# Performance work log

Hardware: AMD Instinct MI355X
Metric: run time of the kernel (lower is better)

## Reference

```python
import jax, jax.numpy as jnp
import numpy as np
from jax import lax

D_MODEL = 512
D_STATE = 16
D_CONV = 4
EXPAND = 2
D_INNER = EXPAND * D_MODEL          # 1024
DT_RANK = int(np.ceil(D_MODEL / 16))  # 32


def setup_inputs() -> dict:
    key = jax.random.key(0)
    ks = jax.random.split(key, 10)
    s = lambda k, shape, sc: (jax.random.normal(k, shape, dtype=jnp.float32) * sc)
    x = jax.random.normal(ks[0], (8, D_MODEL, 128, 128), dtype=jnp.float32)
    W_in = s(ks[1], (2 * D_INNER, D_MODEL), 1.0 / np.sqrt(D_MODEL))
    conv_w = s(ks[2], (D_INNER, D_CONV), 1.0 / np.sqrt(D_CONV))
    conv_b = s(ks[3], (D_INNER,), 0.02)
    W_x = s(ks[4], (DT_RANK + 2 * D_STATE, D_INNER), 1.0 / np.sqrt(D_INNER))
    W_dt = s(ks[5], (D_INNER, DT_RANK), 1.0 / np.sqrt(DT_RANK))
    b_dt = s(ks[6], (D_INNER,), 0.02)
    # S4D-real init: A_log[d, n] = log(n+1)
    A_log = jnp.log(jnp.broadcast_to(jnp.arange(1, D_STATE + 1, dtype=jnp.float32), (D_INNER, D_STATE)))
    D_param = jnp.ones((D_INNER,), dtype=jnp.float32)
    W_out = s(ks[7], (D_MODEL, D_INNER), 1.0 / np.sqrt(D_INNER))
    return {"x": x, "W_in": W_in, "conv_w": conv_w, "conv_b": conv_b,
            "W_x": W_x, "W_dt": W_dt, "b_dt": b_dt, "A_log": A_log,
            "D_param": D_param, "W_out": W_out}


def _mamba(u, W_in, conv_w, conv_b, W_x, W_dt, b_dt, A_log, D_param, W_out):
    # u: (B, L, D_MODEL)
    B, L, _ = u.shape
    xz = jnp.einsum('bld,ed->ble', u, W_in)          # (B, L, 2*D_INNER)
    xp, z = jnp.split(xz, 2, axis=-1)                # each (B, L, D_INNER)
    # causal depthwise conv1d over L
    xc = lax.conv_general_dilated(
        xp.transpose(0, 2, 1), conv_w[:, None, :],
        window_strides=(1,), padding=((D_CONV - 1, 0),),
        dimension_numbers=('NCH', 'OIH', 'NCH'),
        feature_group_count=D_INNER)
    xc = xc[:, :, :L] + conv_b[None, :, None]
    xs = jax.nn.silu(xc.transpose(0, 2, 1))          # (B, L, D_INNER)
    x_dbl = jnp.einsum('bld,ed->ble', xs, W_x)       # (B, L, DT_RANK+2*D_STATE)
    dt, Bm, Cm = jnp.split(x_dbl, [DT_RANK, DT_RANK + D_STATE], axis=-1)
    delta = jax.nn.softplus(jnp.einsum('blr,dr->bld', dt, W_dt) + b_dt)  # (B,L,D_INNER)
    A = -jnp.exp(A_log)                              # (D_INNER, D_STATE)
    dA = jnp.exp(jnp.einsum('bld,dn->bldn', delta, A))
    dBx = jnp.einsum('bld,bln,bld->bldn', delta, Bm, xs)

    def step(h, inp):
        dA_t, dBx_t, C_t = inp
        h = dA_t * h + dBx_t                         # (B, D_INNER, D_STATE)
        y = jnp.einsum('bdn,bn->bd', h, C_t)
        return h, y

    h0 = jnp.zeros((B, D_INNER, D_STATE), dtype=u.dtype)
    _, ys = lax.scan(step, h0, (dA.transpose(1, 0, 2, 3),
                                dBx.transpose(1, 0, 2, 3),
                                Cm.transpose(1, 0, 2)))
    y = ys.transpose(1, 0, 2)                        # (B, L, D_INNER)
    y = y + D_param * xs
    y = y * jax.nn.silu(z)
    return jnp.einsum('bld,ed->ble', y, W_out)       # (B, L, D_MODEL)


def reference(x, W_in, conv_w, conv_b, W_x, W_dt, b_dt, A_log, D_param, W_out):
    # ECA: global avg pool -> (B, 1, C) sequence through Mamba -> sigmoid gate
    y = jnp.mean(x, axis=(2, 3))[:, None, :]         # (B, 1, C)
    y = _mamba(y, W_in, conv_w, conv_b, W_x, W_dt, b_dt, A_log, D_param, W_out)
    gate = jax.nn.sigmoid(y)[:, 0, :, None, None]    # (B, C, 1, 1)
    return x * gate
```

## Files before the change

kernel.cpp:

```cpp
#include <hip/hip_runtime.h>
#include <math.h>

#define DMODEL 512
#define DINNER 1024
#define DTRANK 32
#define DSTATE 16
#define HW     16384
#define BATCH  8

typedef float vf4 __attribute__((ext_vector_type(4)));

__device__ __forceinline__ float wave_reduce(float s) {
#pragma unroll
    for (int off = 32; off; off >>= 1) s += __shfl_xor(s, off);
    return s;
}

__device__ __forceinline__ float dot4(vf4 a, vf4 b) {
    return a.x * b.x + a.y * b.y + a.z * b.z + a.w * b.w;
}

__global__ __launch_bounds__(256) void mean_kernel(const float* __restrict__ x,
                                                   float* __restrict__ mean_out) {
    const int row = blockIdx.x;
    const vf4* xr = (const vf4*)(x + (size_t)row * HW);
    const int t = threadIdx.x;
    float s = 0.f;
#pragma unroll
    for (int j = 0; j < 16; ++j) {
        vf4 v = xr[t + j * 256];
        s += v.x + v.y + v.z + v.w;
    }
    for (int off = 32; off; off >>= 1) s += __shfl_down(s, off);
    __shared__ float part[4];
    if ((t & 63) == 0) part[t >> 6] = s;
    __syncthreads();
    if (t == 0) {
        float tot = part[0] + part[1] + part[2] + part[3];
        mean_out[row] = tot * (1.0f / (float)HW);
    }
}

__global__ __launch_bounds__(256) void k2a_win_kernel(
    const float* __restrict__ mean_in,
    const float* __restrict__ W_in,
    const float* __restrict__ conv_w,
    const float* __restrict__ conv_b,
    float* __restrict__ xs_buf,
    float* __restrict__ sz_buf)
{
    const int e = blockIdx.x;
    const int t = threadIdx.x;
    const int lane = t & 63;
    const int wv = t >> 6;

    const vf4* row = (const vf4*)(W_in + (size_t)e * DMODEL);
    const vf4 w0 = row[lane];
    const vf4 w1 = row[lane + 64];
    const vf4* u4 = (const vf4*)mean_in;

    float acc[2];
#pragma unroll
    for (int k = 0; k < 2; ++k) {
        const int b = wv * 2 + k;
        vf4 a = u4[b * 128 + lane];
        vf4 c = u4[b * 128 + lane + 64];
        acc[k] = dot4(w0, a) + dot4(w1, c);
        acc[k] = wave_reduce(acc[k]);
    }

    if (lane == 0) {
        if (e < DINNER) {
            const float cw = conv_w[e * 4 + 3];
            const float cb = conv_b[e];
#pragma unroll
            for (int k = 0; k < 2; ++k) {
                float xc = acc[k] * cw + cb;
                xs_buf[(wv * 2 + k) * DINNER + e] = xc / (1.f + expf(-xc));
            }
        } else {
            const int d = e - DINNER;
#pragma unroll
            for (int k = 0; k < 2; ++k) {
                float zc = acc[k];
                sz_buf[(wv * 2 + k) * DINNER + d] = zc / (1.f + expf(-zc));
            }
        }
    }
}

__global__ __launch_bounds__(512) void k2b_mid_kernel(
    const float* __restrict__ xs_buf,
    const float* __restrict__ sz_buf,
    const float* __restrict__ W_x,
    const float* __restrict__ W_dt,
    const float* __restrict__ b_dt,
    const float* __restrict__ D_param,
    float* __restrict__ yv_buf)
{
    __shared__ float xs[DINNER];
    __shared__ float xdbl[64];
    const int b = blockIdx.x;
    const int t = threadIdx.x;
    const int lane = t & 63;
    const int wv = t >> 6;

#pragma unroll
    for (int i = 0; i < 2; ++i) xs[t + i * 512] = xs_buf[b * DINNER + t + i * 512];
    __syncthreads();

    const vf4* xs4 = (const vf4*)xs;
    for (int oi = 0; oi < 8; ++oi) {
        const int o = wv * 8 + oi;
        const vf4* wr = (const vf4*)(W_x + (size_t)o * DINNER);
        float acc = 0.f;
#pragma unroll
        for (int j = 0; j < 4; ++j)
            acc += dot4(wr[lane + j * 64], xs4[lane + j * 64]);
        acc = wave_reduce(acc);
        if (lane == 0) xdbl[o] = acc;
    }
    __syncthreads();

    float bc = 0.f;
#pragma unroll
    for (int n = 0; n < DSTATE; ++n)
        bc += xdbl[DTRANK + n] * xdbl[DTRANK + DSTATE + n];

#pragma unroll
    for (int k = 0; k < 2; ++k) {
        const int d = t + k * 512;
        float acc = b_dt[d];
        const vf4* wr = (const vf4*)(W_dt + (size_t)d * DTRANK);
        const vf4* dt4 = (const vf4*)xdbl;
#pragma unroll
        for (int r = 0; r < 8; ++r)
            acc += dot4(wr[r], dt4[r]);
        float delta = (acc > 20.f) ? acc : log1pf(expf(acc));
        yv_buf[b * DINNER + d] =
            (delta * bc + D_param[d]) * xs[d] * sz_buf[b * DINNER + d];
    }
}

__global__ __launch_bounds__(256, 6) void gate_mul_kernel(
    const float* __restrict__ x,
    const float* __restrict__ yv_buf,
    const float* __restrict__ W_out,
    float* __restrict__ out)
{
    const int row = (BATCH * DMODEL - 1) - blockIdx.x;
    const int b = row >> 9;
    const int c = row & 511;
    const int t = threadIdx.x;
    const int lane = t & 63;

    const vf4* wr = (const vf4*)(W_out + (size_t)c * DINNER);
    const vf4* yv = (const vf4*)(yv_buf + (size_t)b * DINNER);
    float acc = 0.f;
#pragma unroll
    for (int j = 0; j < 4; ++j)
        acc += dot4(wr[lane + j * 64], yv[lane + j * 64]);
    acc = wave_reduce(acc);
    const float g = 1.f / (1.f + expf(-acc));

    const vf4* xi = (const vf4*)(x + (size_t)row * HW);
    vf4* oo = (vf4*)(out + (size_t)row * HW);
#pragma unroll 4
    for (int j = 0; j < 16; ++j) {
        vf4 v = xi[t + j * 256] * g;
        __builtin_nontemporal_store(v, &oo[t + j * 256]);
    }
}

extern "C" void kernel_launch(void* const* d_in, const int* in_sizes, int n_in,
                              void* d_out, int out_size, void* d_ws, size_t ws_size,
                              hipStream_t stream) {
    const float* x       = (const float*)d_in[0];
    const float* W_in    = (const float*)d_in[1];
    const float* conv_w  = (const float*)d_in[2];
    const float* conv_b  = (const float*)d_in[3];
    const float* W_x     = (const float*)d_in[4];
    const float* W_dt    = (const float*)d_in[5];
    const float* b_dt    = (const float*)d_in[6];
    const float* D_param = (const float*)d_in[8];
    const float* W_out   = (const float*)d_in[9];
    float* out = (float*)d_out;

    float* mean_buf = (float*)d_ws;
    float* xs_buf   = mean_buf + BATCH * DMODEL;
    float* sz_buf   = xs_buf + BATCH * DINNER;
    float* yv_buf   = sz_buf + BATCH * DINNER;

    mean_kernel<<<BATCH * DMODEL, 256, 0, stream>>>(x, mean_buf);
    k2a_win_kernel<<<2048, 256, 0, stream>>>(mean_buf, W_in, conv_w, conv_b,
                                             xs_buf, sz_buf);
    k2b_mid_kernel<<<BATCH, 512, 0, stream>>>(xs_buf, sz_buf, W_x, W_dt, b_dt,
                                              D_param, yv_buf);
    gate_mul_kernel<<<BATCH * DMODEL, 256, 0, stream>>>(x, yv_buf, W_out, out);
}
```

Measured before the change: 144.5 us.

## Split batch into halves so gate pass rereads input from infinity cache

Processes the batch in two halves, running the mean, projection, mid and gate kernels per half. Each half's input slice is small enough to potentially stay resident in the last-level cache between the mean reduction and the gating multiply, cutting HBM reads. It doubles the number of launches and the small serial projection kernels, and drops the reversed block order and occupancy hint on the gate kernel.

```diff
diff --git a/kernel.cpp b/kernel.cpp
--- a/kernel.cpp
+++ b/kernel.cpp
@@ -7,6 +7,7 @@
 #define DSTATE 16
 #define HW     16384
 #define BATCH  8
+#define HBATCH 4
 
 typedef float vf4 __attribute__((ext_vector_type(4)));
 
@@ -21,8 +22,9 @@
 }
 
 __global__ __launch_bounds__(256) void mean_kernel(const float* __restrict__ x,
-                                                   float* __restrict__ mean_out) {
-    const int row = blockIdx.x;
+                                                   float* __restrict__ mean_out,
+                                                   int b0) {
+    const int row = b0 * DMODEL + blockIdx.x;
     const vf4* xr = (const vf4*)(x + (size_t)row * HW);
     const int t = threadIdx.x;
     float s = 0.f;
@@ -47,44 +49,31 @@
     const float* __restrict__ conv_w,
     const float* __restrict__ conv_b,
     float* __restrict__ xs_buf,
-    float* __restrict__ sz_buf)
+    float* __restrict__ sz_buf,
+    int b0)
 {
     const int e = blockIdx.x;
     const int t = threadIdx.x;
     const int lane = t & 63;
-    const int wv = t >> 6;
+    const int b = b0 + (t >> 6);
 
     const vf4* row = (const vf4*)(W_in + (size_t)e * DMODEL);
     const vf4 w0 = row[lane];
     const vf4 w1 = row[lane + 64];
     const vf4* u4 = (const vf4*)mean_in;
 
-    float acc[2];
-#pragma unroll
-    for (int k = 0; k < 2; ++k) {
-        const int b = wv * 2 + k;
-        vf4 a = u4[b * 128 + lane];
-        vf4 c = u4[b * 128 + lane + 64];
-        acc[k] = dot4(w0, a) + dot4(w1, c);
-        acc[k] = wave_reduce(acc[k]);
-    }
+    vf4 a = u4[b * 128 + lane];
+    vf4 c = u4[b * 128 + lane + 64];
+    float acc = dot4(w0, a) + dot4(w1, c);
+    acc = wave_reduce(acc);
 
     if (lane == 0) {
         if (e < DINNER) {
-            const float cw = conv_w[e * 4 + 3];
-            const float cb = conv_b[e];
-#pragma unroll
-            for (int k = 0; k < 2; ++k) {
-                float xc = acc[k] * cw + cb;
-                xs_buf[(wv * 2 + k) * DINNER + e] = xc / (1.f + expf(-xc));
-            }
+            float xc = acc * conv_w[e * 4 + 3] + conv_b[e];
+            xs_buf[b * DINNER + e] = xc / (1.f + expf(-xc));
         } else {
             const int d = e - DINNER;
-#pragma unroll
-            for (int k = 0; k < 2; ++k) {
-                float zc = acc[k];
-                sz_buf[(wv * 2 + k) * DINNER + d] = zc / (1.f + expf(-zc));
-            }
+            sz_buf[b * DINNER + d] = acc / (1.f + expf(-acc));
         }
     }
 }
@@ -96,11 +85,12 @@
     const float* __restrict__ W_dt,
     const float* __restrict__ b_dt,
     const float* __restrict__ D_param,
-    float* __restrict__ yv_buf)
+    float* __restrict__ yv_buf,
+    int b0)
 {
     __shared__ float xs[DINNER];
     __shared__ float xdbl[64];
-    const int b = blockIdx.x;
+    const int b = b0 + blockIdx.x;
     const int t = threadIdx.x;
     const int lane = t & 63;
     const int wv = t >> 6;
@@ -142,13 +132,14 @@
     }
 }
 
-__global__ __launch_bounds__(256, 6) void gate_mul_kernel(
+__global__ __launch_bounds__(256) void gate_mul_kernel(
     const float* __restrict__ x,
     const float* __restrict__ yv_buf,
     const float* __restrict__ W_out,
-    float* __restrict__ out)
+    float* __restrict__ out,
+    int b0)
 {
-    const int row = (BATCH * DMODEL - 1) - blockIdx.x;
+    const int row = b0 * DMODEL + blockIdx.x;
     const int b = row >> 9;
     const int c = row & 511;
     const int t = threadIdx.x;
@@ -191,10 +182,14 @@
     float* sz_buf   = xs_buf + BATCH * DINNER;
     float* yv_buf   = sz_buf + BATCH * DINNER;
 
-    mean_kernel<<<BATCH * DMODEL, 256, 0, stream>>>(x, mean_buf);
-    k2a_win_kernel<<<2048, 256, 0, stream>>>(mean_buf, W_in, conv_w, conv_b,
-                                             xs_buf, sz_buf);
-    k2b_mid_kernel<<<BATCH, 512, 0, stream>>>(xs_buf, sz_buf, W_x, W_dt, b_dt,
-                                              D_param, yv_buf);
-    gate_mul_kernel<<<BATCH * DMODEL, 256, 0, stream>>>(x, yv_buf, W_out, out);
+    for (int half = 0; half < 2; ++half) {
+        const int b0 = half * HBATCH;
+        mean_kernel<<<HBATCH * DMODEL, 256, 0, stream>>>(x, mean_buf, b0);
+        k2a_win_kernel<<<2048, 256, 0, stream>>>(mean_buf, W_in, conv_w, conv_b,
+                                                 xs_buf, sz_buf, b0);
+        k2b_mid_kernel<<<HBATCH, 512, 0, stream>>>(xs_buf, sz_buf, W_x, W_dt,
+                                                   b_dt, D_param, yv_buf, b0);
+        gate_mul_kernel<<<HBATCH * DMODEL, 256, 0, stream>>>(x, yv_buf, W_out,
+                                                             out, b0);
+    }
 }
```

New measurement: 159.2 us. +10.1%, slower.
